# Kernel optimization log

Measured on AMD Instinct MI355X. Metric: run time of the kernel, lower is better.

## Reference

```python
import jax, jax.numpy as jnp
import numpy as np

D_MODEL = 1024

def setup_inputs() -> dict:
    key = jax.random.key(0)
    ks = jax.random.split(key, 7)
    x = jax.random.normal(ks[0], (4, 4096, D_MODEL), dtype=jnp.float32)
    s = 1.0 / np.sqrt(D_MODEL)
    Wq = jax.random.uniform(ks[1], (D_MODEL, D_MODEL), jnp.float32, -s, s)
    bq = jax.random.uniform(ks[2], (D_MODEL,), jnp.float32, -s, s)
    Wk = jax.random.uniform(ks[3], (D_MODEL, D_MODEL), jnp.float32, -s, s)
    bk = jax.random.uniform(ks[4], (D_MODEL,), jnp.float32, -s, s)
    Wv = jax.random.uniform(ks[5], (D_MODEL, D_MODEL), jnp.float32, -s, s)
    bv = jax.random.uniform(ks[6], (D_MODEL,), jnp.float32, -s, s)
    return {"x": x, "Wq": Wq, "bq": bq, "Wk": Wk, "bk": bk, "Wv": Wv, "bv": bv}

def reference(x, Wq, bq, Wk, bk, Wv, bv):
    # Q, K, V: [b, s, d]
    Q = jnp.einsum('bsd,ed->bse', x, Wq) + bq
    K = jnp.einsum('bsd,ed->bse', x, Wk) + bk
    V = jnp.einsum('bsd,ed->bse', x, Wv) + bv
    scale = 1.0 / jnp.sqrt(jnp.asarray(D_MODEL, dtype=x.dtype))
    scores = jnp.einsum('bqd,bkd->bqk', Q, K) * scale  # [b, s, s]
    attn = jax.nn.softmax(scores, axis=-1)
    return jnp.einsum('bqk,bkd->bqd', attn, V)
```

## Files before the change

kernel.cpp:

```cpp
#include <hip/hip_runtime.h>
#include <stdint.h>
#include <stddef.h>

#define DM 1024
#define SEQ 4096
#define NB 4
#define NTOK (NB*SEQ)

typedef __attribute__((ext_vector_type(8))) short s16x8;
typedef __attribute__((ext_vector_type(4))) float f32x4;

__device__ __forceinline__ unsigned short f2bf(float f) {
  unsigned int u = __float_as_uint(f);
  u += 0x7FFFu + ((u >> 16) & 1u);
  return (unsigned short)(u >> 16);
}

__device__ __forceinline__ f32x4 mfma16(s16x8 a, s16x8 b, f32x4 c) {
  return __builtin_amdgcn_mfma_f32_16x16x32_bf16(a, b, c, 0, 0, 0);
}

__device__ __forceinline__ void gload16(const void* g, void* l) {
  __builtin_amdgcn_global_load_lds((const __attribute__((address_space(1))) unsigned int*)g,
                                   (__attribute__((address_space(3))) unsigned int*)l, 16, 0, 0);
}

__device__ __forceinline__ void xcd_swz(int gx, int gy, int& x, int& y, int& z) {
  int nwg = gx * gy * gridDim.z;
  int bid = blockIdx.x + gx * (blockIdx.y + gy * blockIdx.z);
  int cpx = nwg >> 3;
  int wg = (bid & 7) * cpx + (bid >> 3);
  x = wg % gx; int t = wg / gx; y = t % gy; z = t / gy;
}

__global__ void k_conv(const float* __restrict__ s, unsigned short* __restrict__ d, int n8) {
  int i = blockIdx.x * blockDim.x + threadIdx.x;
  int st = gridDim.x * blockDim.x;
  for (; i < n8; i += st) {
    const f32x4* sp = (const f32x4*)s + (size_t)i * 2;
    f32x4 a = sp[0], b = sp[1];
    s16x8 o;
    o[0] = (short)f2bf(a[0]); o[1] = (short)f2bf(a[1]);
    o[2] = (short)f2bf(a[2]); o[3] = (short)f2bf(a[3]);
    o[4] = (short)f2bf(b[0]); o[5] = (short)f2bf(b[1]);
    o[6] = (short)f2bf(b[2]); o[7] = (short)f2bf(b[3]);
    *((s16x8*)d + i) = o;
  }
}

template<int KD, int BK, int EPI>
__device__ __forceinline__ void gemm_core(
    const unsigned short* __restrict__ A, const unsigned short* __restrict__ B,
    void* __restrict__ outp, int ldc, const float* __restrict__ bias, float scale,
    int mbase, int nbase)
{
  constexpr int NT     = KD / BK;
  constexpr int SLOTS  = BK / 8;
  constexpr int SMASK  = SLOTS - 1;
  constexpr int PASSES = 128 * SLOTS / 256;

  __shared__ unsigned short lds[2][2][128 * BK];
  const int tid = threadIdx.x, lane = tid & 63, wid = tid >> 6;
  const int wr = wid >> 1, wc = wid & 1;
  const int l15 = lane & 15, lg = lane >> 4;

  f32x4 acc[4][4];
  #pragma unroll
  for (int m = 0; m < 4; m++)
    #pragma unroll
    for (int n = 0; n < 4; n++) { acc[m][n][0]=0.f; acc[m][n][1]=0.f; acc[m][n][2]=0.f; acc[m][n][3]=0.f; }

  auto rswz = [](int row) -> int { return (BK == 64) ? (row & 7) : ((row >> 1) & 3); };

  auto stage = [&](int buf, int kt) {
    const int kb_ = kt * BK;
    #pragma unroll
    for (int p = 0; p < PASSES; p++) {
      int s = p * 256 + tid;
      int row = s / SLOTS, sl = (s & SMASK) ^ rswz(row);
      gload16(A + (size_t)(mbase + row) * KD + kb_ + sl * 8, &lds[buf][0][s * 8]);
    }
    #pragma unroll
    for (int p = 0; p < PASSES; p++) {
      int s = p * 256 + tid;
      int row = s / SLOTS, sl = (s & SMASK) ^ rswz(row);
      gload16(B + (size_t)(nbase + row) * KD + kb_ + sl * 8, &lds[buf][1][s * 8]);
    }
  };

  auto compute = [&](int buf) {
    #pragma unroll
    for (int k2 = 0; k2 < BK / 32; k2++) {
      s16x8 af[4], bf[4];
      #pragma unroll
      for (int m = 0; m < 4; m++) {
        int row = wr * 64 + m * 16 + l15;
        int sl = (k2 * 4 + lg) ^ rswz(row);
        af[m] = *(const s16x8*)(&lds[buf][0][0] + row * BK + sl * 8);
      }
      #pragma unroll
      for (int n = 0; n < 4; n++) {
        int row = wc * 64 + n * 16 + l15;
        int sl = (k2 * 4 + lg) ^ rswz(row);
        bf[n] = *(const s16x8*)(&lds[buf][1][0] + row * BK + sl * 8);
      }
      #pragma unroll
      for (int m = 0; m < 4; m++)
        #pragma unroll
        for (int n = 0; n < 4; n++)
          acc[m][n] = mfma16(af[m], bf[n], acc[m][n]);
    }
  };

  stage(0, 0);
  __syncthreads();
  for (int kt = 0; kt < NT; kt++) {
    int cur = kt & 1;
    if (kt < NT - 1) stage(cur ^ 1, kt + 1);
    compute(cur);
    __syncthreads();
  }

  #pragma unroll
  for (int n = 0; n < 4; n++) {
    int col = nbase + wc * 64 + n * 16 + l15;
    float bb = (EPI == 0) ? bias[col] : 0.f;
    #pragma unroll
    for (int m = 0; m < 4; m++) {
      #pragma unroll
      for (int r = 0; r < 4; r++) {
        int row = mbase + wr * 64 + m * 16 + lg * 4 + r;
        float v = acc[m][n][r];
        if (EPI == 0) {
          ((unsigned short*)outp)[(size_t)row * ldc + col] = f2bf(v + bb);
        } else if (EPI == 1) {
          _Float16 h = (_Float16)(v * scale);
          ((unsigned short*)outp)[(size_t)row * ldc + col] = __builtin_bit_cast(unsigned short, h);
        } else {
          ((float*)outp)[(size_t)row * ldc + col] = v;
        }
      }
    }
  }
}

__global__ __launch_bounds__(256, 4) void k_qkv(
    const unsigned short* __restrict__ xb, const unsigned short* __restrict__ wb,
    const float* __restrict__ b0, const float* __restrict__ b1, const float* __restrict__ b2,
    unsigned short* __restrict__ qo, unsigned short* __restrict__ ko, unsigned short* __restrict__ vo)
{
  int x, y, z;
  xcd_swz(8, 128, x, y, z);
  gemm_core<DM, 32, 0>(xb, wb + (size_t)z * DM * DM,
                       (z == 0) ? qo : (z == 1) ? ko : vo, DM,
                       (z == 0) ? b0 : (z == 1) ? b1 : b2, 0.f,
                       y * 128, x * 128);
}

__global__ void k_transpose(const unsigned short* __restrict__ v, unsigned short* __restrict__ vt) {
  __shared__ unsigned short t[64][65];
  const int b = blockIdx.z;
  const int rbase = blockIdx.x * 64;
  const int cbase = blockIdx.y * 64;
  const unsigned short* vb = v + (size_t)b * SEQ * DM;
  unsigned short* vtb = vt + (size_t)b * DM * SEQ;
  const int tid = threadIdx.x;
  #pragma unroll
  for (int it = 0; it < 16; it++) {
    int idx = it * 256 + tid;
    int r = idx >> 6, c = idx & 63;
    t[r][c] = vb[(size_t)(rbase + r) * DM + cbase + c];
  }
  __syncthreads();
  #pragma unroll
  for (int it = 0; it < 16; it++) {
    int idx = it * 256 + tid;
    int oc = idx >> 6, ot = idx & 63;
    vtb[(size_t)(cbase + oc) * SEQ + rbase + ot] = t[ot][oc];
  }
}

__global__ __launch_bounds__(256, 4) void k_sgemm(
    const unsigned short* __restrict__ qb, const unsigned short* __restrict__ kb,
    unsigned short* __restrict__ sc0, unsigned short* __restrict__ sc1, int bb)
{
  int x, y, z;
  xcd_swz(32, 32, x, y, z);
  gemm_core<DM, 32, 1>(qb + (size_t)(bb + z) * SEQ * DM, kb + (size_t)(bb + z) * SEQ * DM,
                       z ? sc1 : sc0, SEQ, nullptr, 0.03125f,
                       y * 128, x * 128);
}

__global__ __launch_bounds__(256) void k_softmax(unsigned short* __restrict__ sc0,
                                                 unsigned short* __restrict__ sc1) {
  unsigned short* sc = blockIdx.z ? sc1 : sc0;
  const int row = blockIdx.x * 4 + (threadIdx.x >> 6);
  const int lane = threadIdx.x & 63;
  unsigned short* rp = sc + (size_t)row * SEQ + lane * 8;

  s16x8 v[8];
  #pragma unroll
  for (int j = 0; j < 8; j++) v[j] = *(const s16x8*)(rp + (size_t)j * 512);

  float f[64];
  float m = -1e30f;
  #pragma unroll
  for (int j = 0; j < 8; j++)
    #pragma unroll
    for (int t = 0; t < 8; t++) {
      float x = (float)__builtin_bit_cast(_Float16, (unsigned short)v[j][t]);
      f[j * 8 + t] = x;
      m = fmaxf(m, x);
    }
  m = fmaxf(m, __shfl_xor(m, 1));  m = fmaxf(m, __shfl_xor(m, 2));
  m = fmaxf(m, __shfl_xor(m, 4));  m = fmaxf(m, __shfl_xor(m, 8));
  m = fmaxf(m, __shfl_xor(m, 16)); m = fmaxf(m, __shfl_xor(m, 32));

  float s = 0.f;
  #pragma unroll
  for (int i = 0; i < 64; i++) { f[i] = __expf(f[i] - m); s += f[i]; }
  s += __shfl_xor(s, 1);  s += __shfl_xor(s, 2);  s += __shfl_xor(s, 4);
  s += __shfl_xor(s, 8);  s += __shfl_xor(s, 16); s += __shfl_xor(s, 32);
  float inv = 1.f / s;

  #pragma unroll
  for (int j = 0; j < 8; j++) {
    s16x8 o;
    #pragma unroll
    for (int t = 0; t < 8; t++) o[t] = (short)f2bf(f[j * 8 + t] * inv);
    *(s16x8*)(rp + (size_t)j * 512) = o;
  }
}

__global__ __launch_bounds__(256, 2) void k_pv(
    const unsigned short* __restrict__ sc0, const unsigned short* __restrict__ sc1,
    const unsigned short* __restrict__ vt, float* __restrict__ out, int bb)
{
  int x, y, z;
  xcd_swz(8, 32, x, y, z);
  gemm_core<SEQ, 64, 2>(z ? sc1 : sc0, vt + (size_t)(bb + z) * DM * SEQ,
                        out + (size_t)(bb + z) * SEQ * DM, DM, nullptr, 1.f,
                        y * 128, x * 128);
}

extern "C" void kernel_launch(void* const* d_in, const int* in_sizes, int n_in,
                              void* d_out, int out_size, void* d_ws, size_t ws_size,
                              hipStream_t stream) {
  const float* x  = (const float*)d_in[0];
  const float* Wq = (const float*)d_in[1];
  const float* bq = (const float*)d_in[2];
  const float* Wk = (const float*)d_in[3];
  const float* bk = (const float*)d_in[4];
  const float* Wv = (const float*)d_in[5];
  const float* bv = (const float*)d_in[6];
  float* out = (float*)d_out;
  char* ws = (char*)d_ws;

  unsigned short* xb = (unsigned short*)(ws);
  unsigned short* wb = (unsigned short*)(ws + 33554432);
  unsigned short* qb = (unsigned short*)(ws + 39845888);
  unsigned short* kb = (unsigned short*)(ws + 73400320);
  unsigned short* vb = (unsigned short*)(ws + 106954752);
  unsigned short* vt = (unsigned short*)(ws + 140509184);
  unsigned short* sc0 = xb;
  unsigned short* sc1 = vb;

  k_conv<<<4096, 256, 0, stream>>>(x, xb, NTOK * DM / 8);
  k_conv<<<512, 256, 0, stream>>>(Wq, wb, DM * DM / 8);
  k_conv<<<512, 256, 0, stream>>>(Wk, wb + DM * DM, DM * DM / 8);
  k_conv<<<512, 256, 0, stream>>>(Wv, wb + 2 * DM * DM, DM * DM / 8);

  k_qkv<<<dim3(8, 128, 3), 256, 0, stream>>>(xb, wb, bq, bk, bv, qb, kb, vb);
  k_transpose<<<dim3(64, 16, 4), 256, 0, stream>>>(vb, vt);

  for (int bb = 0; bb < NB; bb += 2) {
    k_sgemm<<<dim3(32, 32, 2), 256, 0, stream>>>(qb, kb, sc0, sc1, bb);
    k_softmax<<<dim3(1024, 1, 2), 256, 0, stream>>>(sc0, sc1);
    k_pv<<<dim3(8, 32, 2), 256, 0, stream>>>(sc0, sc1, vt, out, bb);
  }
}
```

Baseline: 506.2 us.

## Fuse exp into score GEMM, defer normalization, write V transposed from QKV GEMM

The score GEMM epilogue now applies exp directly, with no max subtraction, and stores bf16. A lightweight row-sum kernel replaces the read-modify-write softmax and writes only inverse sums, and the PV GEMM epilogue scales each output row by that inverse sum. The V projection is computed as W·xᵀ, so it writes the transposed V directly, removing the separate transpose kernel. This cuts one full read/write pass over the score matrix plus the transpose traffic. In exchange, exp without max subtraction risks overflow for large scores, and scores lose precision going from fp16 to bf16.

```diff
diff --git a/kernel.cpp b/kernel.cpp
--- a/kernel.cpp
+++ b/kernel.cpp
@@ -14,6 +14,9 @@
   unsigned int u = __float_as_uint(f);
   u += 0x7FFFu + ((u >> 16) & 1u);
   return (unsigned short)(u >> 16);
+}
+__device__ __forceinline__ float bf2f(unsigned short u) {
+  return __uint_as_float((unsigned int)u << 16);
 }
 
 __device__ __forceinline__ f32x4 mfma16(s16x8 a, s16x8 b, f32x4 c) {
@@ -51,7 +54,7 @@
 template<int KD, int BK, int EPI>
 __device__ __forceinline__ void gemm_core(
     const unsigned short* __restrict__ A, const unsigned short* __restrict__ B,
-    void* __restrict__ outp, int ldc, const float* __restrict__ bias, float scale,
+    void* __restrict__ outp, int ldc, const float* __restrict__ aux, float scale,
     int mbase, int nbase)
 {
   constexpr int NT     = KD / BK;
@@ -124,7 +127,7 @@
   #pragma unroll
   for (int n = 0; n < 4; n++) {
     int col = nbase + wc * 64 + n * 16 + l15;
-    float bb = (EPI == 0) ? bias[col] : 0.f;
+    float cb = (EPI == 0) ? aux[col] : 0.f;
     #pragma unroll
     for (int m = 0; m < 4; m++) {
       #pragma unroll
@@ -132,12 +135,13 @@
         int row = mbase + wr * 64 + m * 16 + lg * 4 + r;
         float v = acc[m][n][r];
         if (EPI == 0) {
-          ((unsigned short*)outp)[(size_t)row * ldc + col] = f2bf(v + bb);
+          ((unsigned short*)outp)[(size_t)row * ldc + col] = f2bf(v + cb);
         } else if (EPI == 1) {
-          _Float16 h = (_Float16)(v * scale);
-          ((unsigned short*)outp)[(size_t)row * ldc + col] = __builtin_bit_cast(unsigned short, h);
+          ((unsigned short*)outp)[(size_t)row * ldc + col] = f2bf(__expf(v * scale));
+        } else if (EPI == 3) {
+          ((unsigned short*)outp)[(size_t)row * ldc + col] = f2bf(v + aux[row]);
         } else {
-          ((float*)outp)[(size_t)row * ldc + col] = v;
+          ((float*)outp)[(size_t)row * ldc + col] = v * aux[row];
         }
       }
     }
@@ -146,37 +150,20 @@
 
 __global__ __launch_bounds__(256, 4) void k_qkv(
     const unsigned short* __restrict__ xb, const unsigned short* __restrict__ wb,
-    const float* __restrict__ b0, const float* __restrict__ b1, const float* __restrict__ b2,
-    unsigned short* __restrict__ qo, unsigned short* __restrict__ ko, unsigned short* __restrict__ vo)
+    const float* __restrict__ b0, const float* __restrict__ b1, const float* __restrict__ bv,
+    unsigned short* __restrict__ qo, unsigned short* __restrict__ ko, unsigned short* __restrict__ vt)
 {
   int x, y, z;
   xcd_swz(8, 128, x, y, z);
-  gemm_core<DM, 32, 0>(xb, wb + (size_t)z * DM * DM,
-                       (z == 0) ? qo : (z == 1) ? ko : vo, DM,
-                       (z == 0) ? b0 : (z == 1) ? b1 : b2, 0.f,
-                       y * 128, x * 128);
-}
-
-__global__ void k_transpose(const unsigned short* __restrict__ v, unsigned short* __restrict__ vt) {
-  __shared__ unsigned short t[64][65];
-  const int b = blockIdx.z;
-  const int rbase = blockIdx.x * 64;
-  const int cbase = blockIdx.y * 64;
-  const unsigned short* vb = v + (size_t)b * SEQ * DM;
-  unsigned short* vtb = vt + (size_t)b * DM * SEQ;
-  const int tid = threadIdx.x;
-  #pragma unroll
-  for (int it = 0; it < 16; it++) {
-    int idx = it * 256 + tid;
-    int r = idx >> 6, c = idx & 63;
-    t[r][c] = vb[(size_t)(rbase + r) * DM + cbase + c];
-  }
-  __syncthreads();
-  #pragma unroll
-  for (int it = 0; it < 16; it++) {
-    int idx = it * 256 + tid;
-    int oc = idx >> 6, ot = idx & 63;
-    vtb[(size_t)(cbase + oc) * SEQ + rbase + ot] = t[ot][oc];
+  if (z < 2) {
+    gemm_core<DM, 32, 0>(xb, wb + (size_t)z * DM * DM,
+                         z ? ko : qo, DM, z ? b1 : b0, 0.f,
+                         y * 128, x * 128);
+  } else {
+    int batch = y >> 5, tokb = (y & 31) * 128;
+    gemm_core<DM, 32, 3>(wb + (size_t)2 * DM * DM, xb + (size_t)batch * SEQ * DM,
+                         vt + (size_t)batch * DM * SEQ, SEQ, bv, 0.f,
+                         x * 128, tokb);
   }
 }
 
@@ -191,55 +178,34 @@
                        y * 128, x * 128);
 }
 
-__global__ __launch_bounds__(256) void k_softmax(unsigned short* __restrict__ sc0,
-                                                 unsigned short* __restrict__ sc1) {
-  unsigned short* sc = blockIdx.z ? sc1 : sc0;
+__global__ __launch_bounds__(256) void k_rowsum(const unsigned short* __restrict__ sc0,
+                                                const unsigned short* __restrict__ sc1,
+                                                float* __restrict__ linv) {
+  const unsigned short* sc = blockIdx.z ? sc1 : sc0;
   const int row = blockIdx.x * 4 + (threadIdx.x >> 6);
   const int lane = threadIdx.x & 63;
-  unsigned short* rp = sc + (size_t)row * SEQ + lane * 8;
-
-  s16x8 v[8];
-  #pragma unroll
-  for (int j = 0; j < 8; j++) v[j] = *(const s16x8*)(rp + (size_t)j * 512);
-
-  float f[64];
-  float m = -1e30f;
-  #pragma unroll
-  for (int j = 0; j < 8; j++)
-    #pragma unroll
-    for (int t = 0; t < 8; t++) {
-      float x = (float)__builtin_bit_cast(_Float16, (unsigned short)v[j][t]);
-      f[j * 8 + t] = x;
-      m = fmaxf(m, x);
-    }
-  m = fmaxf(m, __shfl_xor(m, 1));  m = fmaxf(m, __shfl_xor(m, 2));
-  m = fmaxf(m, __shfl_xor(m, 4));  m = fmaxf(m, __shfl_xor(m, 8));
-  m = fmaxf(m, __shfl_xor(m, 16)); m = fmaxf(m, __shfl_xor(m, 32));
-
+  const unsigned short* rp = sc + (size_t)row * SEQ + lane * 8;
   float s = 0.f;
   #pragma unroll
-  for (int i = 0; i < 64; i++) { f[i] = __expf(f[i] - m); s += f[i]; }
+  for (int j = 0; j < 8; j++) {
+    s16x8 v = *(const s16x8*)(rp + (size_t)j * 512);
+    #pragma unroll
+    for (int t = 0; t < 8; t++) s += bf2f((unsigned short)v[t]);
+  }
   s += __shfl_xor(s, 1);  s += __shfl_xor(s, 2);  s += __shfl_xor(s, 4);
   s += __shfl_xor(s, 8);  s += __shfl_xor(s, 16); s += __shfl_xor(s, 32);
-  float inv = 1.f / s;
-
-  #pragma unroll
-  for (int j = 0; j < 8; j++) {
-    s16x8 o;
-    #pragma unroll
-    for (int t = 0; t < 8; t++) o[t] = (short)f2bf(f[j * 8 + t] * inv);
-    *(s16x8*)(rp + (size_t)j * 512) = o;
-  }
+  if (lane == 0) linv[blockIdx.z * SEQ + row] = 1.f / s;
 }
 
 __global__ __launch_bounds__(256, 2) void k_pv(
     const unsigned short* __restrict__ sc0, const unsigned short* __restrict__ sc1,
-    const unsigned short* __restrict__ vt, float* __restrict__ out, int bb)
+    const unsigned short* __restrict__ vt, const float* __restrict__ linv,
+    float* __restrict__ out, int bb)
 {
   int x, y, z;
   xcd_swz(8, 32, x, y, z);
-  gemm_core<SEQ, 64, 2>(z ? sc1 : sc0, vt + (size_t)(bb + z) * DM * SEQ,
-                        out + (size_t)(bb + z) * SEQ * DM, DM, nullptr, 1.f,
+  gemm_core<SEQ, 64, 4>(z ? sc1 : sc0, vt + (size_t)(bb + z) * DM * SEQ,
+                        out + (size_t)(bb + z) * SEQ * DM, DM, linv + z * SEQ, 1.f,
                         y * 128, x * 128);
 }
 
@@ -260,22 +226,21 @@
   unsigned short* wb = (unsigned short*)(ws + 33554432);
   unsigned short* qb = (unsigned short*)(ws + 39845888);
   unsigned short* kb = (unsigned short*)(ws + 73400320);
-  unsigned short* vb = (unsigned short*)(ws + 106954752);
+  unsigned short* sc1 = (unsigned short*)(ws + 106954752);
   unsigned short* vt = (unsigned short*)(ws + 140509184);
+  float* linv = (float*)(ws + 174063616);
   unsigned short* sc0 = xb;
-  unsigned short* sc1 = vb;
 
   k_conv<<<4096, 256, 0, stream>>>(x, xb, NTOK * DM / 8);
   k_conv<<<512, 256, 0, stream>>>(Wq, wb, DM * DM / 8);
   k_conv<<<512, 256, 0, stream>>>(Wk, wb + DM * DM, DM * DM / 8);
   k_conv<<<512, 256, 0, stream>>>(Wv, wb + 2 * DM * DM, DM * DM / 8);
 
-  k_qkv<<<dim3(8, 128, 3), 256, 0, stream>>>(xb, wb, bq, bk, bv, qb, kb, vb);
-  k_transpose<<<dim3(64, 16, 4), 256, 0, stream>>>(vb, vt);
+  k_qkv<<<dim3(8, 128, 3), 256, 0, stream>>>(xb, wb, bq, bk, bv, qb, kb, vt);
 
   for (int bb = 0; bb < NB; bb += 2) {
     k_sgemm<<<dim3(32, 32, 2), 256, 0, stream>>>(qb, kb, sc0, sc1, bb);
-    k_softmax<<<dim3(1024, 1, 2), 256, 0, stream>>>(sc0, sc1);
-    k_pv<<<dim3(8, 32, 2), 256, 0, stream>>>(sc0, sc1, vt, out, bb);
-  }
-}
+    k_rowsum<<<dim3(1024, 1, 2), 256, 0, stream>>>(sc0, sc1, linv);
+    k_pv<<<dim3(8, 32, 2), 256, 0, stream>>>(sc0, sc1, vt, linv, out, bb);
+  }
+}
```

Result: no change. 511.6 us (+1.1%).
